# Optimization experiments

Hardware: AMD Instinct MI355X
Metric: run time of the kernel (lower is better)

The kernel has to match this reference:

```python
import jax, jax.numpy as jnp
import numpy as np

N_ATOMS = 100000
N_EDGES = 300000
ATOM_DIM = 32
BOND_DIM = 16
STEPS = 4


def setup_inputs() -> dict:
    key = jax.random.key(0)
    ks = jax.random.split(key, 8)
    atom_features = jax.random.normal(ks[0], (N_ATOMS, ATOM_DIM), dtype=jnp.float32)
    bond_features = jax.random.normal(ks[1], (N_EDGES, BOND_DIM), dtype=jnp.float32)
    pair_indices = jax.random.randint(ks[2], (N_EDGES, 2), 0, N_ATOMS, dtype=jnp.int64 if jax.config.jax_enable_x64 else jnp.int32)
    W_bond = jax.random.normal(ks[3], (BOND_DIM, ATOM_DIM * ATOM_DIM), dtype=jnp.float32) * 0.05
    b_bond = jnp.zeros((ATOM_DIM * ATOM_DIM,), dtype=jnp.float32)
    W_ih = jax.random.normal(ks[4], (3 * ATOM_DIM, ATOM_DIM), dtype=jnp.float32) * 0.1
    W_hh = jax.random.normal(ks[5], (3 * ATOM_DIM, ATOM_DIM), dtype=jnp.float32) * 0.1
    b_ih = jnp.zeros((3 * ATOM_DIM,), dtype=jnp.float32)
    b_hh = jnp.zeros((3 * ATOM_DIM,), dtype=jnp.float32)
    return {
        'atom_features': atom_features,
        'bond_features': bond_features,
        'pair_indices': pair_indices,
        'W_bond': W_bond, 'b_bond': b_bond,
        'W_ih': W_ih, 'W_hh': W_hh, 'b_ih': b_ih, 'b_hh': b_hh,
    }


def _gru_cell(x, h, W_ih, W_hh, b_ih, b_hh):
    # torch.nn.GRUCell semantics
    gi = x @ W_ih.T + b_ih  # [N, 3H]
    gh = h @ W_hh.T + b_hh
    i_r, i_z, i_n = jnp.split(gi, 3, axis=-1)
    h_r, h_z, h_n = jnp.split(gh, 3, axis=-1)
    r = jax.nn.sigmoid(i_r + h_r)
    z = jax.nn.sigmoid(i_z + h_z)
    n = jnp.tanh(i_n + r * h_n)
    return (1.0 - z) * n + z * h


def reference(atom_features, bond_features, pair_indices, W_bond, b_bond, W_ih, W_hh, b_ih, b_hh):
    n_atoms, d = atom_features.shape
    # Edge transform matrices (identical every step in the original; hoisted)
    edge_mats = (bond_features @ W_bond + b_bond).reshape(-1, d, d)  # [E, d, d]
    dst = pair_indices[:, 0]
    nbr = pair_indices[:, 1]
    h = atom_features
    for _ in range(STEPS):
        # gather neighbor states, per-edge matvec, scatter-add
        msg = jnp.einsum('eij,ej->ei', edge_mats, h[nbr])  # [E, d]
        agg = jax.ops.segment_sum(msg, dst, num_segments=n_atoms)  # [N, d]
        h = _gru_cell(agg, h, W_ih, W_hh, b_ih, b_hh)
    return h
```

## Files before the change

### kernel.cpp

```cpp
#include <hip/hip_runtime.h>
#include <hip/hip_cooperative_groups.h>

namespace cg = cooperative_groups;

#define NA 100000
#define NE 300000
#define STEPS 4
#define NTILES (NE / 16)
#define ATILES (NA / 16)
#define GBLK 512

typedef _Float16 f16;
typedef _Float16 half8 __attribute__((ext_vector_type(8)));
using f32x4 = __attribute__((ext_vector_type(4))) float;

__global__ __launch_bounds__(256) void setup_kernel(
    const float* __restrict__ atom,
    const float* __restrict__ Wb, const float* __restrict__ bb,
    const float* __restrict__ Wih, const float* __restrict__ Whh,
    f16* __restrict__ hbf, f16* __restrict__ Wbt,
    f16* __restrict__ Wihb, f16* __restrict__ Whhb,
    int* __restrict__ rowcnt, int* __restrict__ total)
{
    int t = blockIdx.x * 256 + threadIdx.x;
    const int NH8 = NA * 32 / 8;
    if (t < NH8) {
        float4 a = reinterpret_cast<const float4*>(atom)[2 * t];
        float4 b = reinterpret_cast<const float4*>(atom)[2 * t + 1];
        half8 o;
        o[0]=(f16)a.x; o[1]=(f16)a.y; o[2]=(f16)a.z; o[3]=(f16)a.w;
        o[4]=(f16)b.x; o[5]=(f16)b.y; o[6]=(f16)b.z; o[7]=(f16)b.w;
        reinterpret_cast<half8*>(hbf)[t] = o;
        return;
    }
    int u = t - NH8;
    if (u < NA) {
        rowcnt[u] = 0;
        if (u == 0) *total = 0;
        return;
    }
    int v = u - NA;
    if (v < 17 * 32 * 32) {
        int j = v & 31, i = (v >> 5) & 31, k = v >> 10;
        float val = (k < 16) ? Wb[k * 1024 + i * 32 + j] : bb[i * 32 + j];
        int row = ((i & 4) ? 16 : 0) + ((i >> 3) << 2) + (i & 3);
        Wbt[(k * 32 + row) * 32 + j] = (f16)val;
    } else if (v < 17 * 32 * 32 + 3072) {
        int q = v - 17 * 32 * 32;
        Wihb[q] = (f16)Wih[q];
    } else if (v < 17 * 32 * 32 + 6144) {
        int q = v - 17 * 32 * 32 - 3072;
        Whhb[q] = (f16)Whh[q];
    }
}

__global__ __launch_bounds__(256) void hist_kernel(
    const int* __restrict__ pair, int* __restrict__ cnt)
{
    int e = blockIdx.x * 256 + threadIdx.x;
    if (e < NE) atomicAdd(&cnt[reinterpret_cast<const int2*>(pair)[e].x], 1);
}

__global__ __launch_bounds__(1024) void alloc_kernel(
    const int* __restrict__ cnt, int* __restrict__ start,
    int* __restrict__ next, int* __restrict__ total)
{
    __shared__ int tmp[1024];
    __shared__ int base;
    int g = blockIdx.x * 1024 + threadIdx.x;
    int v = (g < NA) ? cnt[g] : 0;
    tmp[threadIdx.x] = v;
    __syncthreads();
    for (int off = 1; off < 1024; off <<= 1) {
        int u = (threadIdx.x >= off) ? tmp[threadIdx.x - off] : 0;
        __syncthreads();
        tmp[threadIdx.x] += u;
        __syncthreads();
    }
    if (threadIdx.x == 1023) base = atomicAdd(total, tmp[1023]);
    __syncthreads();
    if (g < NA) {
        int s = base + tmp[threadIdx.x] - v;
        start[g] = s;
        next[g] = s;
    }
}

__global__ __launch_bounds__(256) void scatter_kernel(
    const float* __restrict__ bond, const int* __restrict__ pair,
    int* __restrict__ next, int* __restrict__ nbrp, f16* __restrict__ bondp)
{
    int e = blockIdx.x * 256 + threadIdx.x;
    if (e >= NE) return;
    int2 p = reinterpret_cast<const int2*>(pair)[e];
    int pos = atomicAdd(&next[p.x], 1);
    nbrp[pos] = p.y;
    const float4* b4 = reinterpret_cast<const float4*>(bond + (size_t)e * 16);
    float4 b0 = b4[0], b1 = b4[1], b2 = b4[2], b3 = b4[3];
    half8 o0, o1;
    o0[0]=(f16)b0.x; o0[1]=(f16)b0.y; o0[2]=(f16)b0.z; o0[3]=(f16)b0.w;
    o0[4]=(f16)b1.x; o0[5]=(f16)b1.y; o0[6]=(f16)b1.z; o0[7]=(f16)b1.w;
    o1[0]=(f16)b2.x; o1[1]=(f16)b2.y; o1[2]=(f16)b2.z; o1[3]=(f16)b2.w;
    o1[4]=(f16)b3.x; o1[5]=(f16)b3.y; o1[6]=(f16)b3.z; o1[7]=(f16)b3.w;
    half8* dst = reinterpret_cast<half8*>(bondp + (size_t)pos * 16);
    dst[0] = o0; dst[1] = o1;
}

__device__ __forceinline__ void msg_body(
    const f16* __restrict__ h, const f16* __restrict__ bondp,
    const int* __restrict__ nbrp, const f16* __restrict__ Wbt,
    f16* __restrict__ msgb, int wid, int nw, int col, int kg)
{
    half8 w0[17], w1[17];
#pragma unroll
    for (int t = 0; t < 17; ++t) {
        w0[t] = *reinterpret_cast<const half8*>(Wbt + (t * 32 + col) * 32 + kg * 8);
        w1[t] = *reinterpret_cast<const half8*>(Wbt + (t * 32 + 16 + col) * 32 + kg * 8);
    }
    int tile = wid;
    int pos = 0;
    half8 hf{}, cA{}, cB{};
    if (tile < NTILES) {
        pos = tile * 16 + col;
        int nbr0 = nbrp[pos];
        cA = *reinterpret_cast<const half8*>(bondp + (size_t)pos * 16);
        cB = *reinterpret_cast<const half8*>(bondp + (size_t)pos * 16 + 8);
        hf = *reinterpret_cast<const half8*>(h + (size_t)nbr0 * 32 + kg * 8);
    }
    while (tile < NTILES) {
        int tile2 = tile + nw;
        int pos2 = 0;
        half8 hf2{}, cA2{}, cB2{};
        if (tile2 < NTILES) {
            pos2 = tile2 * 16 + col;
            int nbr2 = nbrp[pos2];
            cA2 = *reinterpret_cast<const half8*>(bondp + (size_t)pos2 * 16);
            cB2 = *reinterpret_cast<const half8*>(bondp + (size_t)pos2 * 16 + 8);
            hf2 = *reinterpret_cast<const half8*>(h + (size_t)nbr2 * 32 + kg * 8);
        }
        f32x4 acc0 = {0.f, 0.f, 0.f, 0.f};
        f32x4 acc1 = {0.f, 0.f, 0.f, 0.f};
#pragma unroll
        for (int t = 0; t < 16; ++t) {
            f16 ch = (t < 8) ? cA[t] : cB[t - 8];
            half8 a = hf * ch;
            acc0 = __builtin_amdgcn_mfma_f32_16x16x32_f16(w0[t], a, acc0, 0, 0, 0);
            acc1 = __builtin_amdgcn_mfma_f32_16x16x32_f16(w1[t], a, acc1, 0, 0, 0);
        }
        acc0 = __builtin_amdgcn_mfma_f32_16x16x32_f16(w0[16], hf, acc0, 0, 0, 0);
        acc1 = __builtin_amdgcn_mfma_f32_16x16x32_f16(w1[16], hf, acc1, 0, 0, 0);

        half8 so;
        so[0]=(f16)acc0[0]; so[1]=(f16)acc0[1]; so[2]=(f16)acc0[2]; so[3]=(f16)acc0[3];
        so[4]=(f16)acc1[0]; so[5]=(f16)acc1[1]; so[6]=(f16)acc1[2]; so[7]=(f16)acc1[3];
        *reinterpret_cast<half8*>(msgb + (size_t)pos * 32 + kg * 8) = so;

        tile = tile2; pos = pos2; hf = hf2; cA = cA2; cB = cB2;
    }
}

__device__ __forceinline__ void gru_body(
    const f16* __restrict__ msgb, const int* __restrict__ start,
    const int* __restrict__ cnt, f16* __restrict__ h,
    const f16* __restrict__ Wihb, const f16* __restrict__ Whhb,
    const float* __restrict__ bih, const float* __restrict__ bhh,
    float* __restrict__ hout, int wf, int wid, int nw, int col, int kg)
{
    half8 wi[6], wh[6];
#pragma unroll
    for (int t = 0; t < 6; ++t) {
        wi[t] = *reinterpret_cast<const half8*>(Wihb + (size_t)(t * 16 + col) * 32 + kg * 8);
        wh[t] = *reinterpret_cast<const half8*>(Whhb + (size_t)(t * 16 + col) * 32 + kg * 8);
    }
    float br0  = bih[col]      + bhh[col];
    float bz0  = bih[32 + col] + bhh[32 + col];
    float bin0 = bih[64 + col];
    float bhn0 = bhh[64 + col];
    float br1  = bih[16 + col] + bhh[16 + col];
    float bz1  = bih[48 + col] + bhh[48 + col];
    float bin1 = bih[80 + col];
    float bhn1 = bhh[80 + col];

    for (int tile = wid; tile < ATILES; tile += nw) {
        int base = tile * 16;
        int a0   = base + col;
        int st = start[a0], en = st + cnt[a0];
        half8 hfrag = *reinterpret_cast<const half8*>(h + (size_t)a0 * 32 + kg * 8);

        float xs[8] = {0.f, 0.f, 0.f, 0.f, 0.f, 0.f, 0.f, 0.f};
        int p = st;
        while (p < en) {
            int n = en - p;
            half8 m0, m1, m2, m3;
            m0 = *reinterpret_cast<const half8*>(msgb + (size_t)p * 32 + kg * 8);
            if (n > 1) m1 = *reinterpret_cast<const half8*>(msgb + (size_t)(p + 1) * 32 + kg * 8);
            if (n > 2) m2 = *reinterpret_cast<const half8*>(msgb + (size_t)(p + 2) * 32 + kg * 8);
            if (n > 3) m3 = *reinterpret_cast<const half8*>(msgb + (size_t)(p + 3) * 32 + kg * 8);
#pragma unroll
            for (int j = 0; j < 8; ++j) xs[j] += (float)m0[j];
            if (n > 1) {
#pragma unroll
                for (int j = 0; j < 8; ++j) xs[j] += (float)m1[j];
            }
            if (n > 2) {
#pragma unroll
                for (int j = 0; j < 8; ++j) xs[j] += (float)m2[j];
            }
            if (n > 3) {
#pragma unroll
                for (int j = 0; j < 8; ++j) xs[j] += (float)m3[j];
            }
            p += 4;
        }
        half8 xfrag;
#pragma unroll
        for (int j = 0; j < 8; ++j) xfrag[j] = (f16)xs[j];

        f32x4 gi[6], gh[6];
#pragma unroll
        for (int t = 0; t < 6; ++t) {
            f32x4 z = {0.f, 0.f, 0.f, 0.f};
            gi[t] = __builtin_amdgcn_mfma_f32_16x16x32_f16(xfrag, wi[t], z, 0, 0, 0);
            gh[t] = __builtin_amdgcn_mfma_f32_16x16x32_f16(hfrag, wh[t], z, 0, 0, 0);
        }

#pragma unroll
        for (int hh = 0; hh < 2; ++hh) {
            float br  = hh ? br1  : br0;
            float bz  = hh ? bz1  : bz0;
            float bin = hh ? bin1 : bin0;
            float bhn = hh ? bhn1 : bhn0;
            int i = hh * 16 + col;
#pragma unroll
            for (int reg = 0; reg < 4; ++reg) {
                int a = base + kg * 4 + reg;
                float r = 1.f / (1.f + __expf(-(gi[hh][reg] + gh[hh][reg] + br)));
                float z = 1.f / (1.f + __expf(-(gi[2 + hh][reg] + gh[2 + hh][reg] + bz)));
                float n = tanhf(gi[4 + hh][reg] + bin + r * (gh[4 + hh][reg] + bhn));
                float hp = (float)h[(size_t)a * 32 + i];
                float o  = (1.f - z) * n + z * hp;
                if (wf) hout[(size_t)a * 32 + i] = o;
                h[(size_t)a * 32 + i] = (f16)o;
            }
        }
    }
}

__global__ __launch_bounds__(256, 2) void msg_kernel(
    const f16* __restrict__ hb, const f16* __restrict__ bondp,
    const int* __restrict__ nbrp, const f16* __restrict__ Wbt,
    f16* __restrict__ msgb)
{
    int wave = threadIdx.x >> 6;
    int lane = threadIdx.x & 63;
    msg_body(hb, bondp, nbrp, Wbt, msgb,
             blockIdx.x * 4 + wave, gridDim.x << 2, lane & 15, lane >> 4);
}

__global__ __launch_bounds__(256) void gru_kernel(
    const f16* __restrict__ msgb, const int* __restrict__ start,
    const int* __restrict__ cnt, f16* __restrict__ hb,
    const f16* __restrict__ Wihb, const f16* __restrict__ Whhb,
    const float* __restrict__ bih, const float* __restrict__ bhh,
    float* __restrict__ hout, int wf)
{
    int wave = threadIdx.x >> 6;
    int lane = threadIdx.x & 63;
    gru_body(msgb, start, cnt, hb, Wihb, Whhb, bih, bhh, hout, wf,
             blockIdx.x * 4 + wave, gridDim.x << 2, lane & 15, lane >> 4);
}

__global__ __launch_bounds__(256, 2) void step_kernel(
    f16* __restrict__ h, const f16* __restrict__ bondp,
    const int* __restrict__ nbrp, const f16* __restrict__ Wbt,
    f16* __restrict__ msgb, const int* __restrict__ start,
    const int* __restrict__ cnt,
    const f16* __restrict__ Wihb, const f16* __restrict__ Whhb,
    const float* __restrict__ bih, const float* __restrict__ bhh,
    float* __restrict__ hout)
{
    cg::grid_group grid = cg::this_grid();
    int wave = threadIdx.x >> 6;
    int lane = threadIdx.x & 63;
    int col  = lane & 15;
    int kg   = lane >> 4;
    int wid  = blockIdx.x * 4 + wave;
    int nw   = gridDim.x << 2;

    for (int s = 0; s < STEPS; ++s) {
        msg_body(h, bondp, nbrp, Wbt, msgb, wid, nw, col, kg);
        grid.sync();
        gru_body(msgb, start, cnt, h, Wihb, Whhb, bih, bhh, hout,
                 (s == STEPS - 1) ? 1 : 0, wid, nw, col, kg);
        grid.sync();
    }
}

extern "C" void kernel_launch(void* const* d_in, const int* in_sizes, int n_in,
                              void* d_out, int out_size, void* d_ws, size_t ws_size,
                              hipStream_t stream)
{
    const float* atom = (const float*)d_in[0];
    const float* bond = (const float*)d_in[1];
    const int*   pair = (const int*)  d_in[2];
    const float* Wb   = (const float*)d_in[3];
    const float* bb   = (const float*)d_in[4];
    const float* W_ih = (const float*)d_in[5];
    const float* W_hh = (const float*)d_in[6];
    const float* b_ih = (const float*)d_in[7];
    const float* b_hh = (const float*)d_in[8];
    float* out = (float*)d_out;

    char* w = (char*)d_ws;
    f16* msg    = (f16*)w;
    f16* hbf    = (f16*)(w + 19200000);
    f16* bondp  = (f16*)(w + 25600000);
    f16* Wbt    = (f16*)(w + 35200000);
    f16* Wihb   = Wbt + 17 * 32 * 32;
    f16* Whhb   = Wihb + 96 * 32;
    int* rowcnt = (int*)(w + 35248000);
    int* startp = (int*)(w + 35648000);
    int* nextp  = (int*)(w + 36048000);
    int* nbrp   = (int*)(w + 36448000);
    int* total  = (int*)(w + 37648000);

    const int setup_threads = NA * 32 / 8 + NA + 17 * 32 * 32 + 6144;
    setup_kernel<<<(setup_threads + 255) / 256, 256, 0, stream>>>(
        atom, Wb, bb, W_ih, W_hh, hbf, Wbt, Wihb, Whhb, rowcnt, total);
    hist_kernel<<<(NE + 255) / 256, 256, 0, stream>>>(pair, rowcnt);
    alloc_kernel<<<(NA + 1023) / 1024, 1024, 0, stream>>>(rowcnt, startp, nextp, total);
    scatter_kernel<<<(NE + 255) / 256, 256, 0, stream>>>(bond, pair, nextp, nbrp, bondp);

    int bpc = 0;
    hipError_t qe = hipOccupancyMaxActiveBlocksPerMultiprocessor(
        &bpc, (const void*)step_kernel, 256, 0);
    if (qe == hipSuccess && bpc >= 2) {
        void* args[12];
        args[0]  = &hbf;   args[1]  = &bondp;  args[2]  = &nbrp;
        args[3]  = &Wbt;   args[4]  = &msg;    args[5]  = &startp;
        args[6]  = &rowcnt; args[7] = &Wihb;   args[8]  = &Whhb;
        args[9]  = (void*)&b_ih; args[10] = (void*)&b_hh; args[11] = &out;
        hipLaunchCooperativeKernel((void*)step_kernel, dim3(GBLK), dim3(256),
                                   args, 0, stream);
    } else {
        const int gru_blocks = (ATILES + 3) / 4;
        for (int s = 0; s < STEPS; ++s) {
            msg_kernel<<<512, 256, 0, stream>>>(hbf, bondp, nbrp, Wbt, msg);
            gru_kernel<<<gru_blocks, 256, 0, stream>>>(msg, startp, rowcnt, hbf,
                                                       Wihb, Whhb, b_ih, b_hh, out,
                                                       (s == STEPS - 1) ? 1 : 0);
        }
    }
}
```

Measured before the change: 195.3 us.

## Fuse message computation into GRU pass with double-buffered hidden state

Replaces the two-phase step (compute all edge messages to a global buffer, grid sync, then aggregate and run the GRU) with a single pass per atom tile. Each tile computes the messages for its own incoming CSR edges with MFMA and reduces them through wave shuffles, and ping-pong hidden-state buffers allow one grid sync per step instead of two. This removes the global message write and re-read plus half the grid barriers. In exchange it adds per-edge shuffle loops, keeps 34 bond-weight fragments in registers, and moves the GRU weights into LDS, so register pressure may lower occupancy or throughput.

```diff
diff --git a/kernel.cpp b/kernel.cpp
--- a/kernel.cpp
+++ b/kernel.cpp
@@ -13,6 +13,13 @@
 typedef _Float16 f16;
 typedef _Float16 half8 __attribute__((ext_vector_type(8)));
 using f32x4 = __attribute__((ext_vector_type(4))) float;
+
+__device__ __forceinline__ float f16lo(unsigned int v) {
+    return (float)__builtin_bit_cast(f16, (unsigned short)(v & 0xffffu));
+}
+__device__ __forceinline__ float f16hi(unsigned int v) {
+    return (float)__builtin_bit_cast(f16, (unsigned short)(v >> 16));
+}
 
 __global__ __launch_bounds__(256) void setup_kernel(
     const float* __restrict__ atom,
@@ -188,29 +195,10 @@
         half8 hfrag = *reinterpret_cast<const half8*>(h + (size_t)a0 * 32 + kg * 8);
 
         float xs[8] = {0.f, 0.f, 0.f, 0.f, 0.f, 0.f, 0.f, 0.f};
-        int p = st;
-        while (p < en) {
-            int n = en - p;
-            half8 m0, m1, m2, m3;
-            m0 = *reinterpret_cast<const half8*>(msgb + (size_t)p * 32 + kg * 8);
-            if (n > 1) m1 = *reinterpret_cast<const half8*>(msgb + (size_t)(p + 1) * 32 + kg * 8);
-            if (n > 2) m2 = *reinterpret_cast<const half8*>(msgb + (size_t)(p + 2) * 32 + kg * 8);
-            if (n > 3) m3 = *reinterpret_cast<const half8*>(msgb + (size_t)(p + 3) * 32 + kg * 8);
-#pragma unroll
-            for (int j = 0; j < 8; ++j) xs[j] += (float)m0[j];
-            if (n > 1) {
-#pragma unroll
-                for (int j = 0; j < 8; ++j) xs[j] += (float)m1[j];
-            }
-            if (n > 2) {
-#pragma unroll
-                for (int j = 0; j < 8; ++j) xs[j] += (float)m2[j];
-            }
-            if (n > 3) {
-#pragma unroll
-                for (int j = 0; j < 8; ++j) xs[j] += (float)m3[j];
-            }
-            p += 4;
+        for (int p = st; p < en; ++p) {
+            half8 m = *reinterpret_cast<const half8*>(msgb + (size_t)p * 32 + kg * 8);
+#pragma unroll
+            for (int j = 0; j < 8; ++j) xs[j] += (float)m[j];
         }
         half8 xfrag;
 #pragma unroll
@@ -223,7 +211,6 @@
             gi[t] = __builtin_amdgcn_mfma_f32_16x16x32_f16(xfrag, wi[t], z, 0, 0, 0);
             gh[t] = __builtin_amdgcn_mfma_f32_16x16x32_f16(hfrag, wh[t], z, 0, 0, 0);
         }
-
 #pragma unroll
         for (int hh = 0; hh < 2; ++hh) {
             float br  = hh ? br1  : br0;
@@ -270,15 +257,23 @@
              blockIdx.x * 4 + wave, gridDim.x << 2, lane & 15, lane >> 4);
 }
 
-__global__ __launch_bounds__(256, 2) void step_kernel(
-    f16* __restrict__ h, const f16* __restrict__ bondp,
-    const int* __restrict__ nbrp, const f16* __restrict__ Wbt,
-    f16* __restrict__ msgb, const int* __restrict__ start,
+__global__ __launch_bounds__(256, 2) void fused_kernel(
+    f16* __restrict__ h0buf, f16* __restrict__ h1buf,
+    const f16* __restrict__ bondp, const int* __restrict__ nbrp,
+    const f16* __restrict__ Wbt, const int* __restrict__ start,
     const int* __restrict__ cnt,
     const f16* __restrict__ Wihb, const f16* __restrict__ Whhb,
     const float* __restrict__ bih, const float* __restrict__ bhh,
     float* __restrict__ hout)
 {
+    __shared__ f16 lwi[96 * 32];
+    __shared__ f16 lwh[96 * 32];
+    for (int t = threadIdx.x; t < 96 * 32 / 8; t += 256) {
+        reinterpret_cast<half8*>(lwi)[t] = reinterpret_cast<const half8*>(Wihb)[t];
+        reinterpret_cast<half8*>(lwh)[t] = reinterpret_cast<const half8*>(Whhb)[t];
+    }
+    __syncthreads();
+
     cg::grid_group grid = cg::this_grid();
     int wave = threadIdx.x >> 6;
     int lane = threadIdx.x & 63;
@@ -287,12 +282,117 @@
     int wid  = blockIdx.x * 4 + wave;
     int nw   = gridDim.x << 2;
 
+    half8 w0[17], w1[17];
+#pragma unroll
+    for (int t = 0; t < 17; ++t) {
+        w0[t] = *reinterpret_cast<const half8*>(Wbt + (t * 32 + col) * 32 + kg * 8);
+        w1[t] = *reinterpret_cast<const half8*>(Wbt + (t * 32 + 16 + col) * 32 + kg * 8);
+    }
+    float br0  = bih[col]      + bhh[col];
+    float bz0  = bih[32 + col] + bhh[32 + col];
+    float bin0 = bih[64 + col];
+    float bhn0 = bhh[64 + col];
+    float br1  = bih[16 + col] + bhh[16 + col];
+    float bz1  = bih[48 + col] + bhh[48 + col];
+    float bin1 = bih[80 + col];
+    float bhn1 = bhh[80 + col];
+
+    f16* hp = h0buf;
+    f16* hn = h1buf;
+
     for (int s = 0; s < STEPS; ++s) {
-        msg_body(h, bondp, nbrp, Wbt, msgb, wid, nw, col, kg);
+        int wf = (s == STEPS - 1);
+        for (int tile = wid; tile < ATILES; tile += nw) {
+            int base = tile * 16;
+            int a0   = base + col;
+            int st = start[a0], en = st + cnt[a0];
+            int tb = __shfl(st, lane & 48);
+            int te = __shfl(en, (lane & 48) | 15);
+
+            float xs[8] = {0.f, 0.f, 0.f, 0.f, 0.f, 0.f, 0.f, 0.f};
+
+            for (int cb = tb; cb < te; cb += 16) {
+                int el = cb + col;
+                int elc = (el < te) ? el : (te - 1);
+                int nbr = nbrp[elc];
+                half8 cA = *reinterpret_cast<const half8*>(bondp + (size_t)elc * 16);
+                half8 cB = *reinterpret_cast<const half8*>(bondp + (size_t)elc * 16 + 8);
+                half8 hf = *reinterpret_cast<const half8*>(hp + (size_t)nbr * 32 + kg * 8);
+
+                f32x4 acc0 = {0.f, 0.f, 0.f, 0.f};
+                f32x4 acc1 = {0.f, 0.f, 0.f, 0.f};
+#pragma unroll
+                for (int t = 0; t < 16; ++t) {
+                    f16 ch = (t < 8) ? cA[t] : cB[t - 8];
+                    half8 a = hf * ch;
+                    acc0 = __builtin_amdgcn_mfma_f32_16x16x32_f16(w0[t], a, acc0, 0, 0, 0);
+                    acc1 = __builtin_amdgcn_mfma_f32_16x16x32_f16(w1[t], a, acc1, 0, 0, 0);
+                }
+                acc0 = __builtin_amdgcn_mfma_f32_16x16x32_f16(w0[16], hf, acc0, 0, 0, 0);
+                acc1 = __builtin_amdgcn_mfma_f32_16x16x32_f16(w1[16], hf, acc1, 0, 0, 0);
+
+                union { half8 hh8; unsigned int u[4]; } pk;
+                pk.hh8[0]=(f16)acc0[0]; pk.hh8[1]=(f16)acc0[1];
+                pk.hh8[2]=(f16)acc0[2]; pk.hh8[3]=(f16)acc0[3];
+                pk.hh8[4]=(f16)acc1[0]; pk.hh8[5]=(f16)acc1[1];
+                pk.hh8[6]=(f16)acc1[2]; pk.hh8[7]=(f16)acc1[3];
+
+                int lo = st > cb ? st : cb;
+                int hi = en < cb + 16 ? en : cb + 16;
+                int mylen = hi - lo; if (mylen < 0) mylen = 0;
+                int rbase = lo - cb;
+                for (int it = 0; it < 16; ++it) {
+                    if (__all(it >= mylen)) break;
+                    int srcl = (lane & 48) | ((rbase + it) & 15);
+                    unsigned int v0 = __shfl(pk.u[0], srcl);
+                    unsigned int v1 = __shfl(pk.u[1], srcl);
+                    unsigned int v2 = __shfl(pk.u[2], srcl);
+                    unsigned int v3 = __shfl(pk.u[3], srcl);
+                    if (it < mylen) {
+                        xs[0] += f16lo(v0); xs[1] += f16hi(v0);
+                        xs[2] += f16lo(v1); xs[3] += f16hi(v1);
+                        xs[4] += f16lo(v2); xs[5] += f16hi(v2);
+                        xs[6] += f16lo(v3); xs[7] += f16hi(v3);
+                    }
+                }
+            }
+
+            half8 xfrag;
+#pragma unroll
+            for (int j = 0; j < 8; ++j) xfrag[j] = (f16)xs[j];
+            half8 hfrag = *reinterpret_cast<const half8*>(hp + (size_t)a0 * 32 + kg * 8);
+
+            f32x4 gi[6], gh[6];
+#pragma unroll
+            for (int t = 0; t < 6; ++t) {
+                half8 wiF = *reinterpret_cast<const half8*>(lwi + (t * 16 + col) * 32 + kg * 8);
+                half8 whF = *reinterpret_cast<const half8*>(lwh + (t * 16 + col) * 32 + kg * 8);
+                f32x4 z = {0.f, 0.f, 0.f, 0.f};
+                gi[t] = __builtin_amdgcn_mfma_f32_16x16x32_f16(xfrag, wiF, z, 0, 0, 0);
+                gh[t] = __builtin_amdgcn_mfma_f32_16x16x32_f16(hfrag, whF, z, 0, 0, 0);
+            }
+#pragma unroll
+            for (int hh = 0; hh < 2; ++hh) {
+                float br  = hh ? br1  : br0;
+                float bz  = hh ? bz1  : bz0;
+                float bin = hh ? bin1 : bin0;
+                float bhn = hh ? bhn1 : bhn0;
+                int i = hh * 16 + col;
+#pragma unroll
+                for (int reg = 0; reg < 4; ++reg) {
+                    int a = base + kg * 4 + reg;
+                    float r = 1.f / (1.f + __expf(-(gi[hh][reg] + gh[hh][reg] + br)));
+                    float z = 1.f / (1.f + __expf(-(gi[2 + hh][reg] + gh[2 + hh][reg] + bz)));
+                    float n = tanhf(gi[4 + hh][reg] + bin + r * (gh[4 + hh][reg] + bhn));
+                    float hpv = (float)hp[(size_t)a * 32 + i];
+                    float o   = (1.f - z) * n + z * hpv;
+                    if (wf) hout[(size_t)a * 32 + i] = o;
+                    hn[(size_t)a * 32 + i] = (f16)o;
+                }
+            }
+        }
         grid.sync();
-        gru_body(msgb, start, cnt, h, Wihb, Whhb, bih, bhh, hout,
-                 (s == STEPS - 1) ? 1 : 0, wid, nw, col, kg);
-        grid.sync();
+        f16* tmp = hp; hp = hn; hn = tmp;
     }
 }
 
@@ -313,6 +413,7 @@
 
     char* w = (char*)d_ws;
     f16* msg    = (f16*)w;
+    f16* h1     = (f16*)w;
     f16* hbf    = (f16*)(w + 19200000);
     f16* bondp  = (f16*)(w + 25600000);
     f16* Wbt    = (f16*)(w + 35200000);
@@ -333,14 +434,14 @@
 
     int bpc = 0;
     hipError_t qe = hipOccupancyMaxActiveBlocksPerMultiprocessor(
-        &bpc, (const void*)step_kernel, 256, 0);
+        &bpc, (const void*)fused_kernel, 256, 0);
     if (qe == hipSuccess && bpc >= 2) {
         void* args[12];
-        args[0]  = &hbf;   args[1]  = &bondp;  args[2]  = &nbrp;
-        args[3]  = &Wbt;   args[4]  = &msg;    args[5]  = &startp;
-        args[6]  = &rowcnt; args[7] = &Wihb;   args[8]  = &Whhb;
+        args[0]  = &hbf;    args[1]  = &h1;     args[2]  = &bondp;
+        args[3]  = &nbrp;   args[4]  = &Wbt;    args[5]  = &startp;
+        args[6]  = &rowcnt; args[7]  = &Wihb;   args[8]  = &Whhb;
         args[9]  = (void*)&b_ih; args[10] = (void*)&b_hh; args[11] = &out;
-        hipLaunchCooperativeKernel((void*)step_kernel, dim3(GBLK), dim3(256),
+        hipLaunchCooperativeKernel((void*)fused_kernel, dim3(GBLK), dim3(256),
                                    args, 0, stream);
     } else {
         const int gru_blocks = (ATILES + 3) / 4;
```

After: 204.5 us. +4.7%, slower.
